# Optimization experiments

Hardware: AMD Instinct MI355X
Metric: run time of the kernel (lower is better)

Reference implementation:

```python
import jax, jax.numpy as jnp
import numpy as np

# samplelist from init_kwargs: coarse node i -> fine nodes (i, i+16)
SAMPLELIST = [[i, i + 16] for i in range(16)]
INDEX = np.array([c for grp in SAMPLELIST for c in grp])  # flattened, len 32
N_NODES = len(SAMPLELIST)   # 16 coarse nodes
KSIZE = 2                   # len of each samplelist group
BATCH, FEAT = 8192, 64      # features == dct_n == input_feature


def setup_inputs() -> dict:
    key = jax.random.key(0)
    k1, k2, k3 = jax.random.split(key, 3)
    x = jax.random.normal(k1, (BATCH, FEAT, 3, N_NODES), dtype=jnp.float32)
    # per-node nn.Linear(3, 3*KSIZE): stacked weights [N, 3k, 3], biases [N, 3k]
    bound = 1.0 / np.sqrt(3.0)
    W = jax.random.uniform(k2, (N_NODES, 3 * KSIZE, 3), jnp.float32, -bound, bound)
    b = jax.random.uniform(k3, (N_NODES, 3 * KSIZE), jnp.float32, -bound, bound)
    return {"x": x, "W": W, "b": b}


def reference(x, W, b):
    B, F, C, N = x.shape  # C == 3
    k = KSIZE
    # Fused block-diagonal matmul replacing the per-node Linear loop:
    # for node n: y_n = x[:,:,:,n] @ W_n^T + b_n  -> [B,F,3k]
    y = jnp.einsum('bfcn,noc->bfno', x, W) + b          # [B,F,N,3k]
    # torch reshape (B*F, 3k) -> (B*F, 3, k): output index o = c*k + m
    # then cat(dim=3) over nodes => last-dim order is node-major: col = n*k + m
    y = y.reshape(B, F, N, 3, k).transpose(0, 1, 3, 2, 4).reshape(B, F, 3, N * k)
    # Faithful replication of the original in-place aliased column reorder
    # (y = y1 then y[..., index[i]] = y1[..., i] sequentially on the SAME buffer).
    # N*k = 32 fixed iterations, tiny fixed loop.
    for i in range(N * k):
        y = y.at[:, :, :, int(INDEX[i])].set(y[:, :, :, i])
    return y
```

## Files before the change

### kernel.cpp

```cpp
#include <hip/hip_runtime.h>


#define BATCH 8192
#define FEAT  64
#define BF_TOTAL (BATCH * FEAT)
#define ROWS_PER_BLOCK 64
#define THREADS 256

__constant__ int c_SRC[32] = {
    0, 2, 4, 6, 8, 10, 12, 14,
    1, 5, 9, 13, 3, 11, 7, 15,
    1, 3, 5, 7, 9, 11, 13, 15,
    3, 7, 11, 15, 7, 15, 15, 31
};

__global__ __launch_bounds__(THREADS)
void GraphUpSample_12120397709982_kernel(const float* __restrict__ x,
                                         const float* __restrict__ W,
                                         const float* __restrict__ bia,
                                         float* __restrict__ out)
{
    __shared__ float  xs[ROWS_PER_BLOCK * 48];
    __shared__ float4 tbl[96];
    __shared__ int    nn[96];

    const int tid = threadIdx.x;
    const long long rowbase = (long long)blockIdx.x * ROWS_PER_BLOCK;

    const float4* xg  = (const float4*)(x + rowbase * 48);
    float4*       xsv = (float4*)xs;
#pragma unroll
    for (int j = 0; j < 3; ++j)
        xsv[tid + j * THREADS] = xg[tid + j * THREADS];

    if (tid < 96) {
        const int c   = tid >> 5;
        const int col = tid & 31;
        const int s   = c_SRC[col];
        const int n   = s >> 1;
        const int o   = c * 2 + (s & 1);
        const float* wp = W + (n * 6 + o) * 3;
        tbl[tid] = make_float4(wp[0], wp[1], wp[2], bia[n * 6 + o]);
        nn[tid]  = n;
    }
    __syncthreads();

    float4* og = (float4*)(out + rowbase * 96);
#pragma unroll
    for (int j = 0; j < 6; ++j) {
        const int p    = tid + j * THREADS;
        const int row  = p / 24;
        const int foff = (p - row * 24) * 4;
        const float* xr = xs + row * 48;
        float4 o4;
        float* o4p = (float*)&o4;
#pragma unroll
        for (int q = 0; q < 4; ++q) {
            const int e = foff + q;
            const int n = nn[e];
            const float4 w = tbl[e];
            o4p[q] = xr[n] * w.x + xr[16 + n] * w.y + xr[32 + n] * w.z + w.w;
        }
        og[p] = o4;
    }
}

extern "C" void kernel_launch(void* const* d_in, const int* in_sizes, int n_in,
                              void* d_out, int out_size, void* d_ws, size_t ws_size,
                              hipStream_t stream) {
    const float* x = (const float*)d_in[0];
    const float* W = (const float*)d_in[1];
    const float* b = (const float*)d_in[2];
    float* out = (float*)d_out;

    const int blocks = BF_TOTAL / ROWS_PER_BLOCK;
    GraphUpSample_12120397709982_kernel<<<blocks, THREADS, 0, stream>>>(x, W, b, out);
}
```

Baseline: 58.26 us.

## Drop shared-memory staging; compute per-column with register weights and nontemporal accesses

Replaces the LDS staging of x and the shared weight table with a per-thread fixed output column: each thread keeps its 3x3 weights and biases in registers and reads the three needed x values directly from global memory. Outputs are written as scalar nontemporal stores, coalesced across the 32 columns, instead of float4 stores. This removes the __syncthreads and the LDS traffic. In exchange it uses narrower scalar loads that re-read x redundantly across threads and scalar stores, which may lower memory efficiency.

```diff
diff --git a/kernel.cpp b/kernel.cpp
--- a/kernel.cpp
+++ b/kernel.cpp
@@ -20,48 +20,40 @@
                                          const float* __restrict__ bia,
                                          float* __restrict__ out)
 {
-    __shared__ float  xs[ROWS_PER_BLOCK * 48];
-    __shared__ float4 tbl[96];
-    __shared__ int    nn[96];
-
-    const int tid = threadIdx.x;
+    const int tid  = threadIdx.x;
+    const int col  = tid & 31;
+    const int rsub = tid >> 5;
     const long long rowbase = (long long)blockIdx.x * ROWS_PER_BLOCK;
 
-    const float4* xg  = (const float4*)(x + rowbase * 48);
-    float4*       xsv = (float4*)xs;
+    const int s = c_SRC[col];
+    const int n = s >> 1;
+    const int m = s & 1;
+
+    float w[3][3], bb[3];
 #pragma unroll
-    for (int j = 0; j < 3; ++j)
-        xsv[tid + j * THREADS] = xg[tid + j * THREADS];
+    for (int c = 0; c < 3; ++c) {
+        const int o = 2 * c + m;
+        const float* wp = W + (n * 6 + o) * 3;
+        w[c][0] = wp[0]; w[c][1] = wp[1]; w[c][2] = wp[2];
+        bb[c] = bia[n * 6 + o];
+    }
 
-    if (tid < 96) {
-        const int c   = tid >> 5;
-        const int col = tid & 31;
-        const int s   = c_SRC[col];
-        const int n   = s >> 1;
-        const int o   = c * 2 + (s & 1);
-        const float* wp = W + (n * 6 + o) * 3;
-        tbl[tid] = make_float4(wp[0], wp[1], wp[2], bia[n * 6 + o]);
-        nn[tid]  = n;
-    }
-    __syncthreads();
+    const float* xb = x   + rowbase * 48;
+    float*       ob = out + rowbase * 96;
 
-    float4* og = (float4*)(out + rowbase * 96);
 #pragma unroll
-    for (int j = 0; j < 6; ++j) {
-        const int p    = tid + j * THREADS;
-        const int row  = p / 24;
-        const int foff = (p - row * 24) * 4;
-        const float* xr = xs + row * 48;
-        float4 o4;
-        float* o4p = (float*)&o4;
+    for (int it = 0; it < ROWS_PER_BLOCK / 8; ++it) {
+        const int row = it * 8 + rsub;
+        const float x0 = __builtin_nontemporal_load(xb + row * 48 +      n);
+        const float x1 = __builtin_nontemporal_load(xb + row * 48 + 16 + n);
+        const float x2 = __builtin_nontemporal_load(xb + row * 48 + 32 + n);
 #pragma unroll
-        for (int q = 0; q < 4; ++q) {
-            const int e = foff + q;
-            const int n = nn[e];
-            const float4 w = tbl[e];
-            o4p[q] = xr[n] * w.x + xr[16 + n] * w.y + xr[32 + n] * w.z + w.w;
+        for (int c = 0; c < 3; ++c) {
+            const float v = fmaf(x0, w[c][0],
+                            fmaf(x1, w[c][1],
+                            fmaf(x2, w[c][2], bb[c])));
+            __builtin_nontemporal_store(v, ob + row * 96 + c * 32 + col);
         }
-        og[p] = o4;
     }
 }
 
```

Measured after the change: 74.30 us. +27.5%, slower.
